# Performance work log

Hardware: AMD Instinct MI355X
Metric: run time of the kernel (lower is better)

Reference implementation:

```python
import jax, jax.numpy as jnp
import numpy as np

WEIGHT = 4.0
SIGMA_DATA = 16.0
ALPHA_DNA = 5.0
ALPHA_RNA = 5.0
ALPHA_LIG = 10.0
EPS = 1e-6
D, L, NTOK = 4, 4096, 512


def setup_inputs() -> dict:
    key = jax.random.key(0)
    ks = jax.random.split(key, 8)
    X_L = jax.random.normal(ks[0], (D, L, 3), dtype=jnp.float32)
    X_gt_L = jax.random.normal(ks[1], (1, L, 3), dtype=jnp.float32)
    crd_mask_L = jax.random.randint(ks[2], (1, L), 0, 2).astype(bool)
    is_dna = jax.random.randint(ks[3], (NTOK,), 0, 2).astype(bool)
    is_rna = jax.random.randint(ks[4], (NTOK,), 0, 2).astype(bool)
    is_ligand = jax.random.randint(ks[5], (NTOK,), 0, 2).astype(bool)
    tok_idx = jnp.sort(jax.random.randint(ks[6], (L,), 0, NTOK, dtype=jnp.int64))
    t = jax.random.uniform(ks[7], (D,), dtype=jnp.float32)
    return {"X_L": X_L, "X_gt_L": X_gt_L, "crd_mask_L": crd_mask_L,
            "is_dna": is_dna, "is_rna": is_rna, "is_ligand": is_ligand,
            "tok_idx": tok_idx, "t": t}


def _smoothed_lddt(X_L, X_gt, crd_mask_L, is_dna, is_rna, tok_idx):
    # X_gt: nan_to_num'd ground truth, shape [1, L, 3]
    n = X_L.shape[1]
    fi, si = jnp.triu_indices(n, k=1)  # P pairs
    gt_d = jnp.linalg.norm(X_gt[0, fi] - X_gt[0, si], axis=-1)  # [P]
    is_na = (is_dna | is_rna)[tok_idx][fi]
    cutoff = jnp.where(is_na, 30.0, 15.0)
    pm = (gt_d > 0) & (gt_d < cutoff)
    pm = pm & crd_mask_L[0, fi] & crd_mask_L[0, si]
    pm = pm & (tok_idx[fi] != tok_idx[si])
    pmf = pm.astype(X_L.dtype)  # [P]
    pred_d = jnp.linalg.norm(X_L[:, fi] - X_L[:, si], axis=-1)  # [D, P]
    delta = jnp.abs(pred_d - gt_d[None, :] + EPS)
    s = (jax.nn.sigmoid(0.5 - delta) + jax.nn.sigmoid(1.0 - delta)
         + jax.nn.sigmoid(2.0 - delta) + jax.nn.sigmoid(4.0 - delta))
    lddt = 0.25 * jnp.sum(s * pmf[None, :], axis=1) / (jnp.sum(pmf) + EPS)
    return 1.0 - lddt  # [D]


def reference(X_L, X_gt_L, crd_mask_L, is_dna, is_rna, is_ligand, tok_idx, t):
    dtype = X_L.dtype
    mask = crd_mask_L.astype(dtype)  # [1, L]
    alpha = (is_dna * ALPHA_DNA + is_rna * ALPHA_RNA + is_ligand * ALPHA_LIG)
    w_L = (1.0 + alpha[tok_idx]).astype(dtype)[None, :] * mask  # [1,L]->[D,L] by bcast
    X_gt = jnp.nan_to_num(X_gt_L)
    sq = jnp.sum((X_L - X_gt) ** 2, axis=-1)  # [D, L]
    l_mse = (1.0 / 3.0) * jnp.sum(w_L * sq, axis=-1) / (jnp.sum(mask[0]) + 1e-4)
    lam = (t ** 2 + SIGMA_DATA ** 2) / ((t * SIGMA_DATA) ** 2)  # edm_lambda
    l_diff = jnp.minimum(lam * l_mse, 2.0)  # clamp_diffusion_loss
    lddt_loss = _smoothed_lddt(X_L, X_gt, crd_mask_L, is_dna, is_rna, tok_idx)
    total = jnp.mean(l_diff) + jnp.mean(lddt_loss)
    return WEIGHT * total
```

## Files before the change

kernel.cpp:

```cpp
#include <hip/hip_runtime.h>

#define LPTS 4096
#define NTOKS 512
#define TILE 32
#define CAP (LPTS + TILE)
#define GRID_B 2080
#define PREP_B 16

#define LOG2E   1.44269504f
#define EPS_S   (1e-6f * LOG2E)
#define CLAMP_S (25.f * LOG2E)
#define CUT15_S (15.f * LOG2E)
#define CUT30_S (30.f * LOG2E)
#define PAD_BIG 1e15f

#define OFF_GT 512
#define OFF_PX (OFF_GT + CAP * 16)
#define OFF_PY (OFF_PX + CAP * 16)
#define OFF_PZ (OFF_PY + CAP * 16)
#define OFF_PART (OFF_PZ + CAP * 16)

static __device__ __forceinline__ float nan0(float x) {
  if (!(x == x)) return 0.f;
  return fminf(fmaxf(x, -3.402823466e38f), 3.402823466e38f);
}

static __device__ __forceinline__ float sterm(float dx, float dy, float dz, float tmp) {
  float d2 = fmaf(dx, dx, fmaf(dy, dy, dz * dz));
  float pd = __builtin_amdgcn_sqrtf(d2);
  float delta = fminf(fabsf(pd + tmp), CLAMP_S);
  float e = __builtin_amdgcn_exp2f(delta);
  float e2 = e * e;
  float e3 = e2 * e;
  float e4 = e2 * e2;
  float Nn = fmaf(0.0366994762f, e3, fmaf(0.7506558488f, e2, fmaf(3.3841830690f, e, 4.f)));
  float Dd = fmaf(0.00055308437f, e4,
             fmaf(0.0366994762f, e3, fmaf(0.3753279244f, e2, fmaf(1.1280610231f, e, 1.f))));
  return Nn * __builtin_amdgcn_rcpf(Dd);
}

__global__ __launch_bounds__(256) void prep_kernel(
    const float* __restrict__ XL, const float* __restrict__ Xgt,
    const void* __restrict__ crd, const void* __restrict__ dna,
    const void* __restrict__ rna, const void* __restrict__ lig,
    const void* __restrict__ tok, float* __restrict__ ws) {
  int b = blockIdx.x, t = threadIdx.x;
  int l = b * 256 + t;
  int* wsi = (int*)ws;
  const int* toki = (const int*)tok;
  const int* crdi = (const int*)crd;
  const unsigned char* crdB = (const unsigned char*)crd;
  __shared__ int sflags[5];
  if (t < 5) sflags[t] = 0;
  __syncthreads();
  {
    int f0 = 0;
    for (int i = t; i < LPTS / 2; i += 256) f0 |= (toki[2 * i + 1] != 0);
    if (f0) atomicOr(&sflags[0], 1);
    int f1 = 0;
    for (int i = t; i < LPTS / 4; i += 256) f1 |= ((unsigned)crdi[i] > 1u);
    if (f1) atomicOr(&sflags[1], 1);
    if (t < NTOKS / 4) {
      if ((unsigned)((const int*)dna)[t] > 1u) atomicOr(&sflags[2], 1);
      if ((unsigned)((const int*)rna)[t] > 1u) atomicOr(&sflags[3], 1);
      if ((unsigned)((const int*)lig)[t] > 1u) atomicOr(&sflags[4], 1);
    }
  }
  __syncthreads();
  bool tok64 = sflags[0] == 0;
  bool crdb = sflags[1] != 0, dnab = sflags[2] != 0,
       rnab = sflags[3] != 0, ligb = sflags[4] != 0;

  int pre = 0;
  for (int i = t; i < b * 256; i += 256)
    pre += crdb ? (crdB[i] != 0) : (crdi[i] != 0);

  int tk = tok64 ? toki[2 * l] : toki[l];
  int tki = min(max(tk, 0), NTOKS - 1);
  int m  = crdb ? (crdB[l] != 0) : (crdi[l] != 0);
  int dn = (dnab ? (int)((const unsigned char*)dna)[tki] : ((const int*)dna)[tki]) != 0;
  int rn = (rnab ? (int)((const unsigned char*)rna)[tki] : ((const int*)rna)[tki]) != 0;
  int lg = (ligb ? (int)((const unsigned char*)lig)[tki] : ((const int*)lig)[tki]) != 0;
  float w = (1.f + 5.f * dn + 5.f * rn + 10.f * lg) * (float)m;
  float gx = nan0(Xgt[3 * l + 0]);
  float gy = nan0(Xgt[3 * l + 1]);
  float gz = nan0(Xgt[3 * l + 2]);
  int meta = (tk & 0xFFFF) | ((dn | rn) << 16);
  float xs[4], ys[4], zs[4];
  float v[5];
#pragma unroll
  for (int d = 0; d < 4; ++d) {
    xs[d] = XL[(d * LPTS + l) * 3 + 0];
    ys[d] = XL[(d * LPTS + l) * 3 + 1];
    zs[d] = XL[(d * LPTS + l) * 3 + 2];
    float dx = xs[d] - gx, dy = ys[d] - gy, dz = zs[d] - gz;
    v[d] = w * (dx * dx + dy * dy + dz * dz);
  }
  v[4] = (float)m;

  int lane = t & 63, wid = t >> 6;
  unsigned long long bal = __ballot(m != 0);
  int p = pre;
#pragma unroll
  for (int off = 32; off; off >>= 1) p += __shfl_down(p, off, 64);
  __shared__ int sw[4], wcnt[4];
  if (lane == 0) { sw[wid] = p; wcnt[wid] = __popcll(bal); }
  __syncthreads();
  int block_base = sw[0] + sw[1] + sw[2] + sw[3];
  int wbase = block_base;
  for (int q = 0; q < wid; ++q) wbase += wcnt[q];
  int pos = wbase + __popcll(bal & ((1ull << lane) - 1ull));
  float4* cgt4 = (float4*)((char*)ws + OFF_GT);
  float4* cpx  = (float4*)((char*)ws + OFF_PX);
  float4* cpy  = (float4*)((char*)ws + OFF_PY);
  float4* cpz  = (float4*)((char*)ws + OFF_PZ);
  if (m) {
    cgt4[pos] = make_float4(gx * LOG2E, gy * LOG2E, gz * LOG2E, __int_as_float(meta));
    cpx[pos] = make_float4(xs[0] * LOG2E, xs[1] * LOG2E, xs[2] * LOG2E, xs[3] * LOG2E);
    cpy[pos] = make_float4(ys[0] * LOG2E, ys[1] * LOG2E, ys[2] * LOG2E, ys[3] * LOG2E);
    cpz[pos] = make_float4(zs[0] * LOG2E, zs[1] * LOG2E, zs[2] * LOG2E, zs[3] * LOG2E);
  }
  if (b == PREP_B - 1) {
    int Lv = block_base + wcnt[0] + wcnt[1] + wcnt[2] + wcnt[3];
    if (t == 0) wsi[5] = Lv;
    if (t < TILE) {
      cgt4[Lv + t] = make_float4(PAD_BIG, PAD_BIG, PAD_BIG, __int_as_float(0x7FFFFFFF));
      float4 z = make_float4(0.f, 0.f, 0.f, 0.f);
      cpx[Lv + t] = z; cpy[Lv + t] = z; cpz[Lv + t] = z;
    }
  }
#pragma unroll
  for (int k = 0; k < 5; ++k) {
    float x = v[k];
#pragma unroll
    for (int off = 32; off; off >>= 1) x += __shfl_down(x, off, 64);
    v[k] = x;
  }
  __shared__ float bred[4][5];
  if (lane == 0)
    for (int k = 0; k < 5; ++k) bred[wid][k] = v[k];
  __syncthreads();
  if (t == 0)
    for (int k = 0; k < 5; ++k)
      ws[8 + b * 5 + k] = bred[0][k] + bred[1][k] + bred[2][k] + bred[3][k];
}

__global__ __launch_bounds__(128) void pair_kernel(float* __restrict__ ws) {
  const int* wsi = (const int*)ws;
  const int Lv = wsi[5];
  const int NT = (Lv + TILE - 1) >> 5;
  const int NA = NT * (NT + 1) / 2;
  const float4* cgt4 = (const float4*)((const char*)ws + OFF_GT);
  const float4* cpx  = (const float4*)((const char*)ws + OFF_PX);
  const float4* cpy  = (const float4*)((const char*)ws + OFF_PY);
  const float4* cpz  = (const float4*)((const char*)ws + OFF_PZ);
  __shared__ float4 sg[TILE], sx[TILE], sy[TILE], sz[TILE];
  __shared__ float bred[2][5];
  int t = threadIdx.x;
  int r = t & 31, g = t >> 5;
  float a0 = 0.f, a1 = 0.f, a2 = 0.f, a3 = 0.f, a4 = 0.f;
  for (int b = blockIdx.x; b < NA; b += GRID_B) {
    int tj = (int)((__builtin_amdgcn_sqrtf(8.f * (float)b + 1.f) - 1.f) * 0.5f);
    while ((tj + 1) * (tj + 2) / 2 <= b) ++tj;
    while (tj * (tj + 1) / 2 > b) --tj;
    int ti = b - tj * (tj + 1) / 2;
    int i0 = ti * TILE, j0 = tj * TILE;
    __syncthreads();
    if (t < 32) sg[t] = cgt4[j0 + t];
    else if (t < 64) sx[t - 32] = cpx[j0 + t - 32];
    else if (t < 96) sy[t - 64] = cpy[j0 + t - 64];
    else sz[t - 96] = cpz[j0 + t - 96];
    __syncthreads();
    int i = i0 + r;
    float4 rg = cgt4[i], rx = cpx[i], ry = cpy[i], rz = cpz[i];
    int rmeta = __float_as_int(rg.w);
    float cutoff = (rmeta & 0x10000) ? CUT30_S : CUT15_S;
    bool diag = (ti == tj);
#pragma unroll
    for (int k = 0; k < 8; ++k) {
      int jj = g * 8 + k;
      float4 cg = sg[jj];
      float dgx = rg.x - cg.x, dgy = rg.y - cg.y, dgz = rg.z - cg.z;
      float gd = __builtin_amdgcn_sqrtf(fmaf(dgx, dgx, fmaf(dgy, dgy, dgz * dgz)));
      bool pm = (gd > 0.f) & (gd < cutoff) & (rmeta != __float_as_int(cg.w));
      if (diag) pm = pm & (jj > r);
      float pmf = pm ? 1.f : 0.f;
      float tmp = EPS_S - gd;
      float4 cx = sx[jj], cy = sy[jj], cz = sz[jj];
      float s0 = sterm(rx.x - cx.x, ry.x - cy.x, rz.x - cz.x, tmp);
      float s1 = sterm(rx.y - cx.y, ry.y - cy.y, rz.y - cz.y, tmp);
      float s2 = sterm(rx.z - cx.z, ry.z - cy.z, rz.z - cz.z, tmp);
      float s3 = sterm(rx.w - cx.w, ry.w - cy.w, rz.w - cz.w, tmp);
      a0 = fmaf(s0, pmf, a0);
      a1 = fmaf(s1, pmf, a1);
      a2 = fmaf(s2, pmf, a2);
      a3 = fmaf(s3, pmf, a3);
      a4 += pmf;
    }
  }
  float v[5] = {a0, a1, a2, a3, a4};
#pragma unroll
  for (int k = 0; k < 5; ++k) {
    float x = v[k];
#pragma unroll
    for (int off = 32; off; off >>= 1) x += __shfl_down(x, off, 64);
    v[k] = x;
  }
  int wid = t >> 6, lane = t & 63;
  if (lane == 0)
    for (int k = 0; k < 5; ++k) bred[wid][k] = v[k];
  __syncthreads();
  if (t == 0) {
    float* part = (float*)((char*)ws + OFF_PART);
#pragma unroll
    for (int k = 0; k < 5; ++k)
      part[blockIdx.x * 5 + k] = bred[0][k] + bred[1][k];
  }
}

__global__ __launch_bounds__(256) void final_kernel(
    const float* __restrict__ ws, const float* __restrict__ t_in,
    float* __restrict__ out) {
  int t = threadIdx.x;
  const float* part = (const float*)((const char*)ws + OFF_PART);
  float u[5] = {0.f, 0.f, 0.f, 0.f, 0.f};
  for (int i = t; i < GRID_B; i += 256) {
#pragma unroll
    for (int k = 0; k < 5; ++k) u[k] += part[i * 5 + k];
  }
#pragma unroll
  for (int k = 0; k < 5; ++k) {
    float x = u[k];
#pragma unroll
    for (int off = 32; off; off >>= 1) x += __shfl_down(x, off, 64);
    u[k] = x;
  }
  __shared__ float bred[4][5];
  int wid = t >> 6, lane = t & 63;
  if (lane == 0)
    for (int k = 0; k < 5; ++k) bred[wid][k] = u[k];
  __syncthreads();
  if (t == 0) {
    float ssum[5];
#pragma unroll
    for (int k = 0; k < 5; ++k)
      ssum[k] = bred[0][k] + bred[1][k] + bred[2][k] + bred[3][k];
    float mse[4] = {0.f, 0.f, 0.f, 0.f};
    float mask_sum = 0.f;
    for (int b = 0; b < PREP_B; ++b) {
#pragma unroll
      for (int d = 0; d < 4; ++d) mse[d] += ws[8 + b * 5 + d];
      mask_sum += ws[8 + b * 5 + 4];
    }
    float pm_sum = ssum[4];
    float tot = 0.f;
#pragma unroll
    for (int d = 0; d < 4; ++d) {
      float lmse = (mse[d] * (1.f / 3.f)) / (mask_sum + 1e-4f);
      float td = t_in[d];
      float lam = (td * td + 256.f) / (256.f * td * td);
      float ldiff = fminf(lam * lmse, 2.f);
      float lddt = 0.25f * ssum[d] / (pm_sum + 1e-6f);
      tot += 0.25f * (ldiff + (1.f - lddt));
    }
    out[0] = 4.f * tot;
  }
}

extern "C" void kernel_launch(void* const* d_in, const int* in_sizes, int n_in,
                              void* d_out, int out_size, void* d_ws, size_t ws_size,
                              hipStream_t stream) {
  (void)in_sizes; (void)n_in; (void)out_size; (void)ws_size;
  const float* XL  = (const float*)d_in[0];
  const float* Xgt = (const float*)d_in[1];
  float* ws = (float*)d_ws;
  float* out = (float*)d_out;
  prep_kernel<<<PREP_B, 256, 0, stream>>>(XL, Xgt, d_in[2], d_in[3], d_in[4],
                                          d_in[5], d_in[6], ws);
  pair_kernel<<<GRID_B, 128, 0, stream>>>(ws);
  final_kernel<<<1, 256, 0, stream>>>(ws, (const float*)d_in[7], out);
}
```

Measured before the change: 26.39 us.

## Replace sigmoid-sum math with shared-memory lookup table and widen pair blocks

The four-sigmoid sum, previously a rational function of exp2, now comes from a 513-entry table with linear interpolation. The table is built in prep_kernel and staged into shared memory by each pair block, with coordinates prescaled so table indices land on a 1/40.96 grid. Pair blocks grow from 128 to 256 threads, each handling 4 columns instead of 8, and the final reduction moves to 1024 threads over a column-major partial layout. This swaps exp, rcp and FMA work for LDS gathers, at the cost of possible bank conflicts and an interpolation error that may exceed tolerance.

After: 28.54 us. +8.2%, slower.

```diff
diff --git a/kernel.cpp b/kernel.cpp
--- a/kernel.cpp
+++ b/kernel.cpp
@@ -7,36 +7,22 @@
 #define GRID_B 2080
 #define PREP_B 16
 
-#define LOG2E   1.44269504f
-#define EPS_S   (1e-6f * LOG2E)
-#define CLAMP_S (25.f * LOG2E)
-#define CUT15_S (15.f * LOG2E)
-#define CUT30_S (30.f * LOG2E)
+#define KSC     40.96f
+#define EPS_K   (1e-6f * KSC)
+#define CUT15_K (15.f * KSC)
+#define CUT30_K (30.f * KSC)
 #define PAD_BIG 1e15f
 
 #define OFF_GT 512
 #define OFF_PX (OFF_GT + CAP * 16)
 #define OFF_PY (OFF_PX + CAP * 16)
 #define OFF_PZ (OFF_PY + CAP * 16)
-#define OFF_PART (OFF_PZ + CAP * 16)
+#define OFF_LUT (OFF_PZ + CAP * 16)
+#define OFF_PART (OFF_LUT + 2112)
 
 static __device__ __forceinline__ float nan0(float x) {
   if (!(x == x)) return 0.f;
   return fminf(fmaxf(x, -3.402823466e38f), 3.402823466e38f);
-}
-
-static __device__ __forceinline__ float sterm(float dx, float dy, float dz, float tmp) {
-  float d2 = fmaf(dx, dx, fmaf(dy, dy, dz * dz));
-  float pd = __builtin_amdgcn_sqrtf(d2);
-  float delta = fminf(fabsf(pd + tmp), CLAMP_S);
-  float e = __builtin_amdgcn_exp2f(delta);
-  float e2 = e * e;
-  float e3 = e2 * e;
-  float e4 = e2 * e2;
-  float Nn = fmaf(0.0366994762f, e3, fmaf(0.7506558488f, e2, fmaf(3.3841830690f, e, 4.f)));
-  float Dd = fmaf(0.00055308437f, e4,
-             fmaf(0.0366994762f, e3, fmaf(0.3753279244f, e2, fmaf(1.1280610231f, e, 1.f))));
-  return Nn * __builtin_amdgcn_rcpf(Dd);
 }
 
 __global__ __launch_bounds__(256) void prep_kernel(
@@ -50,6 +36,15 @@
   const int* toki = (const int*)tok;
   const int* crdi = (const int*)crd;
   const unsigned char* crdB = (const unsigned char*)crd;
+  if (b == 0) {
+    float* lut = (float*)((char*)ws + OFF_LUT);
+    for (int q = t; q <= 512; q += 256) {
+      float d = (float)q / KSC;
+      float s = 1.f / (1.f + __expf(d - 0.5f)) + 1.f / (1.f + __expf(d - 1.f)) +
+                1.f / (1.f + __expf(d - 2.f)) + 1.f / (1.f + __expf(d - 4.f));
+      lut[q] = s;
+    }
+  }
   __shared__ int sflags[5];
   if (t < 5) sflags[t] = 0;
   __syncthreads();
@@ -115,10 +110,10 @@
   float4* cpy  = (float4*)((char*)ws + OFF_PY);
   float4* cpz  = (float4*)((char*)ws + OFF_PZ);
   if (m) {
-    cgt4[pos] = make_float4(gx * LOG2E, gy * LOG2E, gz * LOG2E, __int_as_float(meta));
-    cpx[pos] = make_float4(xs[0] * LOG2E, xs[1] * LOG2E, xs[2] * LOG2E, xs[3] * LOG2E);
-    cpy[pos] = make_float4(ys[0] * LOG2E, ys[1] * LOG2E, ys[2] * LOG2E, ys[3] * LOG2E);
-    cpz[pos] = make_float4(zs[0] * LOG2E, zs[1] * LOG2E, zs[2] * LOG2E, zs[3] * LOG2E);
+    cgt4[pos] = make_float4(gx * KSC, gy * KSC, gz * KSC, __int_as_float(meta));
+    cpx[pos] = make_float4(xs[0] * KSC, xs[1] * KSC, xs[2] * KSC, xs[3] * KSC);
+    cpy[pos] = make_float4(ys[0] * KSC, ys[1] * KSC, ys[2] * KSC, ys[3] * KSC);
+    cpz[pos] = make_float4(zs[0] * KSC, zs[1] * KSC, zs[2] * KSC, zs[3] * KSC);
   }
   if (b == PREP_B - 1) {
     int Lv = block_base + wcnt[0] + wcnt[1] + wcnt[2] + wcnt[3];
@@ -145,7 +140,7 @@
       ws[8 + b * 5 + k] = bred[0][k] + bred[1][k] + bred[2][k] + bred[3][k];
 }
 
-__global__ __launch_bounds__(128) void pair_kernel(float* __restrict__ ws) {
+__global__ __launch_bounds__(256) void pair_kernel(float* __restrict__ ws) {
   const int* wsi = (const int*)ws;
   const int Lv = wsi[5];
   const int NT = (Lv + TILE - 1) >> 5;
@@ -154,10 +149,15 @@
   const float4* cpx  = (const float4*)((const char*)ws + OFF_PX);
   const float4* cpy  = (const float4*)((const char*)ws + OFF_PY);
   const float4* cpz  = (const float4*)((const char*)ws + OFF_PZ);
+  const float* glut  = (const float*)((const char*)ws + OFF_LUT);
   __shared__ float4 sg[TILE], sx[TILE], sy[TILE], sz[TILE];
-  __shared__ float bred[2][5];
+  __shared__ float slut[513];
+  __shared__ float bred[4][5];
   int t = threadIdx.x;
   int r = t & 31, g = t >> 5;
+  slut[t] = glut[t];
+  slut[t + 256] = glut[t + 256];
+  if (t == 0) slut[512] = glut[512];
   float a0 = 0.f, a1 = 0.f, a2 = 0.f, a3 = 0.f, a4 = 0.f;
   for (int b = blockIdx.x; b < NA; b += GRID_B) {
     int tj = (int)((__builtin_amdgcn_sqrtf(8.f * (float)b + 1.f) - 1.f) * 0.5f);
@@ -169,32 +169,42 @@
     if (t < 32) sg[t] = cgt4[j0 + t];
     else if (t < 64) sx[t - 32] = cpx[j0 + t - 32];
     else if (t < 96) sy[t - 64] = cpy[j0 + t - 64];
-    else sz[t - 96] = cpz[j0 + t - 96];
+    else if (t < 128) sz[t - 96] = cpz[j0 + t - 96];
     __syncthreads();
     int i = i0 + r;
     float4 rg = cgt4[i], rx = cpx[i], ry = cpy[i], rz = cpz[i];
     int rmeta = __float_as_int(rg.w);
-    float cutoff = (rmeta & 0x10000) ? CUT30_S : CUT15_S;
+    float cutoff = (rmeta & 0x10000) ? CUT30_K : CUT15_K;
     bool diag = (ti == tj);
 #pragma unroll
-    for (int k = 0; k < 8; ++k) {
-      int jj = g * 8 + k;
+    for (int k = 0; k < 4; ++k) {
+      int jj = g * 4 + k;
       float4 cg = sg[jj];
       float dgx = rg.x - cg.x, dgy = rg.y - cg.y, dgz = rg.z - cg.z;
-      float gd = __builtin_amdgcn_sqrtf(fmaf(dgx, dgx, fmaf(dgy, dgy, dgz * dgz)));
+      float gd = __builtin_amdgcn_sqrtf(
+          fmaxf(fmaf(dgx, dgx, fmaf(dgy, dgy, dgz * dgz)), 0.f));
       bool pm = (gd > 0.f) & (gd < cutoff) & (rmeta != __float_as_int(cg.w));
       if (diag) pm = pm & (jj > r);
       float pmf = pm ? 1.f : 0.f;
-      float tmp = EPS_S - gd;
+      float tmp = EPS_K - gd;
       float4 cx = sx[jj], cy = sy[jj], cz = sz[jj];
-      float s0 = sterm(rx.x - cx.x, ry.x - cy.x, rz.x - cz.x, tmp);
-      float s1 = sterm(rx.y - cx.y, ry.y - cy.y, rz.y - cz.y, tmp);
-      float s2 = sterm(rx.z - cx.z, ry.z - cy.z, rz.z - cz.z, tmp);
-      float s3 = sterm(rx.w - cx.w, ry.w - cy.w, rz.w - cz.w, tmp);
-      a0 = fmaf(s0, pmf, a0);
-      a1 = fmaf(s1, pmf, a1);
-      a2 = fmaf(s2, pmf, a2);
-      a3 = fmaf(s3, pmf, a3);
+#pragma unroll
+      for (int d = 0; d < 4; ++d) {
+        float dx = ((const float*)&rx)[d] - ((const float*)&cx)[d];
+        float dy = ((const float*)&ry)[d] - ((const float*)&cy)[d];
+        float dz = ((const float*)&rz)[d] - ((const float*)&cz)[d];
+        float d2 = fmaxf(fmaf(dx, dx, fmaf(dy, dy, dz * dz)), 0.f);
+        float pd = __builtin_amdgcn_sqrtf(d2);
+        float x = fminf(fabsf(pd + tmp), 511.0f);
+        int ix = (int)x;
+        float fx = x - (float)ix;
+        float lo = slut[ix], hi = slut[ix + 1];
+        float s = fmaf(fx, hi - lo, lo);
+        if (d == 0) a0 = fmaf(s, pmf, a0);
+        else if (d == 1) a1 = fmaf(s, pmf, a1);
+        else if (d == 2) a2 = fmaf(s, pmf, a2);
+        else a3 = fmaf(s, pmf, a3);
+      }
       a4 += pmf;
     }
   }
@@ -214,20 +224,19 @@
     float* part = (float*)((char*)ws + OFF_PART);
 #pragma unroll
     for (int k = 0; k < 5; ++k)
-      part[blockIdx.x * 5 + k] = bred[0][k] + bred[1][k];
-  }
-}
-
-__global__ __launch_bounds__(256) void final_kernel(
+      part[k * GRID_B + blockIdx.x] = bred[0][k] + bred[1][k] + bred[2][k] + bred[3][k];
+  }
+}
+
+__global__ __launch_bounds__(1024) void final_kernel(
     const float* __restrict__ ws, const float* __restrict__ t_in,
     float* __restrict__ out) {
   int t = threadIdx.x;
   const float* part = (const float*)((const char*)ws + OFF_PART);
   float u[5] = {0.f, 0.f, 0.f, 0.f, 0.f};
-  for (int i = t; i < GRID_B; i += 256) {
-#pragma unroll
-    for (int k = 0; k < 5; ++k) u[k] += part[i * 5 + k];
-  }
+#pragma unroll
+  for (int k = 0; k < 5; ++k)
+    for (int i = t; i < GRID_B; i += 1024) u[k] += part[k * GRID_B + i];
 #pragma unroll
   for (int k = 0; k < 5; ++k) {
     float x = u[k];
@@ -235,7 +244,7 @@
     for (int off = 32; off; off >>= 1) x += __shfl_down(x, off, 64);
     u[k] = x;
   }
-  __shared__ float bred[4][5];
+  __shared__ float bred[16][5];
   int wid = t >> 6, lane = t & 63;
   if (lane == 0)
     for (int k = 0; k < 5; ++k) bred[wid][k] = u[k];
@@ -243,8 +252,11 @@
   if (t == 0) {
     float ssum[5];
 #pragma unroll
-    for (int k = 0; k < 5; ++k)
-      ssum[k] = bred[0][k] + bred[1][k] + bred[2][k] + bred[3][k];
+    for (int k = 0; k < 5; ++k) {
+      float x = 0.f;
+      for (int q = 0; q < 16; ++q) x += bred[q][k];
+      ssum[k] = x;
+    }
     float mse[4] = {0.f, 0.f, 0.f, 0.f};
     float mask_sum = 0.f;
     for (int b = 0; b < PREP_B; ++b) {
@@ -277,6 +289,6 @@
   float* out = (float*)d_out;
   prep_kernel<<<PREP_B, 256, 0, stream>>>(XL, Xgt, d_in[2], d_in[3], d_in[4],
                                           d_in[5], d_in[6], ws);
-  pair_kernel<<<GRID_B, 128, 0, stream>>>(ws);
-  final_kernel<<<1, 256, 0, stream>>>(ws, (const float*)d_in[7], out);
-}
+  pair_kernel<<<GRID_B, 256, 0, stream>>>(ws);
+  final_kernel<<<1, 1024, 0, stream>>>(ws, (const float*)d_in[7], out);
+}
```
